# Kernel optimization log

Hardware: AMD Instinct MI355X
Metric: run time of the kernel (lower is better)

The kernel has to match this reference:

```python
import jax, jax.numpy as jnp
import numpy as np

N = 100_000   # nodes
E = 1_600_000 # edges (avg degree 16)
D = 32        # input = hidden = output channels (module defaults)
L = 3         # num_layers


def setup_inputs() -> dict:
    key = jax.random.key(0)
    ks = jax.random.split(key, 6)
    X = jax.random.normal(ks[0], (N, D), jnp.float32)
    edge_index = jax.random.randint(ks[1], (2, E), 0, N)
    edge_weight = jax.random.uniform(ks[2], (E,), jnp.float32)
    # 8 GCNConv layers per GConvLSTM: x_i, h_i, x_f, h_f, x_c, h_c, x_o, h_o
    conv_w = jax.random.normal(ks[3], (L, 8, D, D), jnp.float32) * np.float32(1.0 / np.sqrt(D))
    conv_b = jnp.zeros((L, 8, D), jnp.float32)
    # peephole weights w_c_i, w_c_f, w_c_o (glorot) and biases b_i, b_f, b_c, b_o (zeros)
    wc = jax.random.normal(ks[4], (L, 3, D), jnp.float32) * np.float32(0.1)
    bg = jnp.zeros((L, 4, D), jnp.float32)
    return dict(X=X, edge_index=edge_index, edge_weight=edge_weight,
                conv_w=conv_w, conv_b=conv_b, wc=wc, bg=bg)


def _gcn_norm(edge_index, edge_weight, n):
    # PyG gcn_norm (sym): add self loops with weight 1, then D^-1/2 A D^-1/2
    loop = jnp.arange(n)
    src = jnp.concatenate([edge_index[0], loop])
    dst = jnp.concatenate([edge_index[1], loop])
    w = jnp.concatenate([edge_weight, jnp.ones((n,), edge_weight.dtype)])
    deg = jax.ops.segment_sum(w, dst, num_segments=n)
    dinv = jnp.where(deg > 0, jax.lax.rsqrt(deg), jnp.zeros_like(deg))
    return src, dst, dinv[src] * w * dinv[dst]


def reference(X, edge_index, edge_weight, conv_w, conv_b, wc, bg):
    n = X.shape[0]
    src, dst, nw = _gcn_norm(edge_index, edge_weight, n)

    def gcn(x, W, b):
        xw = x @ W                                   # [N, D] linear transform
        agg = jax.ops.segment_sum(nw[:, None] * xw[src], dst, num_segments=n)
        return agg + b

    out = X
    for l in range(conv_w.shape[0]):
        x = out
        H = jnp.zeros((n, conv_w.shape[-1]), x.dtype)  # hidden state init (None -> zeros)
        C = jnp.zeros_like(H)                          # cell state init
        Wl, bl = conv_w[l], conv_b[l]
        I = jax.nn.sigmoid(gcn(x, Wl[0], bl[0]) + gcn(H, Wl[1], bl[1]) + wc[l, 0] * C + bg[l, 0])
        F = jax.nn.sigmoid(gcn(x, Wl[2], bl[2]) + gcn(H, Wl[3], bl[3]) + wc[l, 1] * C + bg[l, 1])
        T = jnp.tanh(gcn(x, Wl[4], bl[4]) + gcn(H, Wl[5], bl[5]) + bg[l, 2])
        C = F * C + I * T
        O = jax.nn.sigmoid(gcn(x, Wl[6], bl[6]) + gcn(H, Wl[7], bl[7]) + wc[l, 2] * C + bg[l, 3])
        out = O * jnp.tanh(C)
    return out
```

## Files before the change

### kernel.cpp

```cpp
#include <hip/hip_runtime.h>
#include <math.h>

#define TPB 256
#define NBMAX 2048

__device__ __forceinline__ float fsig(float x) {
    return __builtin_amdgcn_rcpf(1.f + __expf(-x));
}
__device__ __forceinline__ float ftanh(float x) {
    float t = __expf(2.f * fabsf(x));
    float r = 1.f - 2.f * __builtin_amdgcn_rcpf(t + 1.f);
    return copysignf(r, x);
}

__global__ __launch_bounds__(256) void k_zero(int* __restrict__ p, int n) {
    int i = blockIdx.x * 256 + threadIdx.x;
    if (i < n) p[i] = 0;
}


__global__ __launch_bounds__(256) void k_bhist(const int* __restrict__ ei,
                                               int* __restrict__ bhist, int E, int NB) {
    __shared__ int h[NBMAX];
    for (int i = threadIdx.x; i < NB; i += 256) h[i] = 0;
    __syncthreads();
    int stride = gridDim.x * 256;
    for (int e = blockIdx.x * 256 + threadIdx.x; e < E; e += stride)
        atomicAdd(&h[ei[E + e] >> 8], 1);
    __syncthreads();
    for (int i = threadIdx.x; i < NB; i += 256) if (h[i]) atomicAdd(&bhist[i], h[i]);
}

__global__ __launch_bounds__(256) void k_bscan(const int* __restrict__ bhist,
                                               int* __restrict__ bbase, int* __restrict__ bfill,
                                               int* __restrict__ row_start,
                                               int NB, int N, int E) {
    __shared__ int tsum[256];
    int tid = threadIdx.x;
    int per = (NB + 255) / 256;
    int loc[8]; int tot = 0;
    int base = tid * per;
#pragma unroll
    for (int j = 0; j < 8; j++) {
        int i = base + j;
        int v = (j < per && i < NB) ? bhist[i] : 0;
        loc[j] = v; tot += v;
    }
    tsum[tid] = tot;
    __syncthreads();
    for (int off = 1; off < 256; off <<= 1) {
        int t = (tid >= off) ? tsum[tid - off] : 0;
        __syncthreads();
        tsum[tid] += t;
        __syncthreads();
    }
    int run = tsum[tid] - tot;
#pragma unroll
    for (int j = 0; j < 8; j++) {
        int i = base + j;
        if (j < per && i < NB) { bbase[i] = run; bfill[i] = run; run += loc[j]; }
    }
    if (tid == 0) { bbase[NB] = E; row_start[N] = E; }
}

__global__ __launch_bounds__(256) void k_bin(const int* __restrict__ ei,
                                             const float* __restrict__ ew,
                                             int* bfill, int2* __restrict__ ebuf,
                                             int E, int NB) {
    __shared__ int h[NBMAX];
    __shared__ int gb[NBMAX];
    const int EPT = 16;
    int tid = threadIdx.x;
    int base = blockIdx.x * 256 * EPT;
    for (int i = tid; i < NB; i += 256) h[i] = 0;
    __syncthreads();
    int src[EPT]; float w[EPT]; int bkt[EPT]; int lrank[EPT];
#pragma unroll
    for (int j = 0; j < EPT; j++) {
        int e = base + j * 256 + tid;
        if (e < E) {
            src[j] = ei[e]; int d = ei[E + e]; w[j] = ew[e];
            int b = d >> 8;
            bkt[j] = b | ((d & 255) << 16);
            lrank[j] = atomicAdd(&h[b], 1);
        } else bkt[j] = -1;
    }
    __syncthreads();
    for (int i = tid; i < NB; i += 256) gb[i] = h[i] ? atomicAdd(&bfill[i], h[i]) : 0;
    __syncthreads();
#pragma unroll
    for (int j = 0; j < EPT; j++) {
        if (bkt[j] >= 0) {
            int b = bkt[j] & 0xFFFF, dlow = (bkt[j] >> 16) & 0xFF;
            int2 v; v.x = src[j] | (dlow << 24); v.y = __float_as_int(w[j]);
            ebuf[gb[b] + lrank[j]] = v;
        }
    }
}

__global__ __launch_bounds__(256) void k_bucket(const int2* __restrict__ ebuf,
                                                const int* __restrict__ bbase,
                                                int2* __restrict__ csr,
                                                int* __restrict__ row_start,
                                                float* __restrict__ dinv,
                                                const float4* __restrict__ X4,
                                                float4* __restrict__ Y4,
                                                int N, int E) {
    __shared__ int lcnt[256];
    __shared__ float wsum[256];
    __shared__ int lstart[256];
    __shared__ int sc[256];
    __shared__ float sdinv[256];
    int b = blockIdx.x, tid = threadIdx.x;
    int beg = bbase[b], end = bbase[b + 1];
    lcnt[tid] = 0; wsum[tid] = 0.f;
    __syncthreads();
    for (int i = beg + tid; i < end; i += 256) {
        int2 v = ebuf[i];
        int dlow = ((unsigned)v.x) >> 24;
        atomicAdd(&lcnt[dlow], 1);
        atomicAdd(&wsum[dlow], __int_as_float(v.y));
    }
    __syncthreads();
    int myc = lcnt[tid];
    sc[tid] = myc;
    __syncthreads();
    for (int off = 1; off < 256; off <<= 1) {
        int t = (tid >= off) ? sc[tid - off] : 0;
        __syncthreads();
        sc[tid] += t;
        __syncthreads();
    }
    lstart[tid] = sc[tid] - myc;
    int node = (b << 8) + tid;
    float dv = rsqrtf(1.0f + wsum[tid]);
    sdinv[tid] = dv;
    if (node < N) {
        row_start[node] = beg + sc[tid] - myc;
        dinv[node] = dv;
    }
    lcnt[tid] = 0;
    __syncthreads();
    for (int i = beg + tid; i < end; i += 256) {
        int2 v = ebuf[i];
        int dlow = ((unsigned)v.x) >> 24;
        int pos = lstart[dlow] + atomicAdd(&lcnt[dlow], 1);
        int2 o; o.x = v.x & 0x00FFFFFF; o.y = v.y;
        csr[beg + pos] = o;
    }
    int nNodes = N - (b << 8); if (nNodes > 256) nNodes = 256;
    int limit = nNodes * 8;
    size_t base4 = ((size_t)b << 8) * 8;
    for (int i = tid; i < limit; i += 256) {
        float4 v = X4[base4 + i];
        float d = sdinv[i >> 3];
        float4 o; o.x = v.x * d; o.y = v.y * d; o.z = v.z * d; o.w = v.w * d;
        Y4[base4 + i] = o;
    }
}


__global__ __launch_bounds__(256) void k_gather(const float4* __restrict__ Y4,
                                                const int* __restrict__ row_start,
                                                const int2* __restrict__ csr,
                                                const float* __restrict__ dinv,
                                                float4* __restrict__ AX4, int N, int E) {
    int wid = (blockIdx.x * blockDim.x + threadIdx.x) >> 6;
    if (wid >= N) return;
    int lane = threadIdx.x & 63;
    int q = lane >> 3, c4 = lane & 7;
    int rs = row_start[wid], re = row_start[wid + 1];
    float di = dinv[wid];
    float4 self = Y4[(size_t)wid * 8 + c4];
    int e0 = rs + q;
    int2 p[4];
#pragma unroll
    for (int j = 0; j < 4; j++) {
        int e = e0 + j * 8;
        p[j] = csr[e < E ? e : 0];
    }
    float4 y[4]; float w[4];
#pragma unroll
    for (int j = 0; j < 4; j++) {
        int e = e0 + j * 8;
        w[j] = (e < re) ? __int_as_float(p[j].y) : 0.f;
        int s = p[j].x;
        y[j] = Y4[(size_t)(e < re ? s : wid) * 8 + c4];
    }
    float4 acc1, acc2;
    if (q == 0) acc1 = self; else { acc1.x = acc1.y = acc1.z = acc1.w = 0.f; }
    acc2.x = acc2.y = acc2.z = acc2.w = 0.f;
    acc1.x += w[0] * y[0].x; acc1.y += w[0] * y[0].y; acc1.z += w[0] * y[0].z; acc1.w += w[0] * y[0].w;
    acc2.x += w[1] * y[1].x; acc2.y += w[1] * y[1].y; acc2.z += w[1] * y[1].z; acc2.w += w[1] * y[1].w;
    acc1.x += w[2] * y[2].x; acc1.y += w[2] * y[2].y; acc1.z += w[2] * y[2].z; acc1.w += w[2] * y[2].w;
    acc2.x += w[3] * y[3].x; acc2.y += w[3] * y[3].y; acc2.z += w[3] * y[3].z; acc2.w += w[3] * y[3].w;
    for (int e = e0 + 32; e < re; e += 8) {
        int2 t = csr[e];
        float4 yt = Y4[(size_t)t.x * 8 + c4];
        float wt = __int_as_float(t.y);
        acc1.x += wt * yt.x; acc1.y += wt * yt.y; acc1.z += wt * yt.z; acc1.w += wt * yt.w;
    }
    acc1.x += acc2.x; acc1.y += acc2.y; acc1.z += acc2.z; acc1.w += acc2.w;
#pragma unroll
    for (int off = 8; off <= 32; off <<= 1) {
        acc1.x += __shfl_xor(acc1.x, off);
        acc1.y += __shfl_xor(acc1.y, off);
        acc1.z += __shfl_xor(acc1.z, off);
        acc1.w += __shfl_xor(acc1.w, off);
    }
    if (lane < 8) {
        float4 o; o.x = acc1.x * di; o.y = acc1.y * di; o.z = acc1.z * di; o.w = acc1.w * di;
        AX4[(size_t)wid * 8 + c4] = o;
    }
}

__global__ __launch_bounds__(256) void k_gates(const float* __restrict__ AX,
                                               const float* __restrict__ cw,
                                               const float* __restrict__ cb,
                                               const float* __restrict__ wc,
                                               const float* __restrict__ bg,
                                               const float* __restrict__ dinv,
                                               float* __restrict__ outRaw,
                                               float* __restrict__ outY,
                                               int N, int l, int isLast) {
    __shared__ float Ws[32][96];
    __shared__ float Xs[32][33];
    __shared__ float Gs[32][96];
    __shared__ float bS[96];
    __shared__ float wcs[32];
    int tid = threadIdx.x;
    for (int i = tid; i < 3072; i += 256) {
        int k = i / 96, ccol = i - k * 96;
        int g = ccol >> 5, o = ccol & 31;
        int j = (g == 0) ? 0 : ((g == 1) ? 4 : 6);
        Ws[k][ccol] = cw[(((l * 8 + j) * 32) + k) * 32 + o];
    }
    if (tid < 32) {
        int c = tid;
        bS[c]      = cb[((l * 8 + 0) * 32) + c] + cb[((l * 8 + 1) * 32) + c] + bg[((l * 4 + 0) * 32) + c];
        bS[32 + c] = cb[((l * 8 + 4) * 32) + c] + cb[((l * 8 + 5) * 32) + c] + bg[((l * 4 + 2) * 32) + c];
        bS[64 + c] = cb[((l * 8 + 6) * 32) + c] + cb[((l * 8 + 7) * 32) + c] + bg[((l * 4 + 3) * 32) + c];
        wcs[c]     = wc[((l * 3 + 2) * 32) + c];
    }
    int row0 = blockIdx.x * 32;
    for (int i = tid; i < 1024; i += 256) {
        int r = i >> 5, k = i & 31; int gr = row0 + r;
        Xs[r][k] = (gr < N) ? AX[(size_t)gr * 32 + k] : 0.f;
    }
    __syncthreads();
    {
        int r = tid >> 3, g8 = tid & 7;
        float acc[12];
#pragma unroll
        for (int j = 0; j < 12; j++) acc[j] = 0.f;
#pragma unroll
        for (int k = 0; k < 32; k++) {
            float xv = Xs[r][k];
#pragma unroll
            for (int j = 0; j < 12; j++) acc[j] += xv * Ws[k][g8 * 12 + j];
        }
#pragma unroll
        for (int j = 0; j < 12; j++) Gs[r][g8 * 12 + j] = acc[j];
    }
    __syncthreads();
    for (int i = tid; i < 1024; i += 256) {
        int r = i >> 5, c = i & 31;
        int gn = row0 + r;
        if (gn >= N) continue;
        float I = fsig(Gs[r][c] + bS[c]);
        float T = ftanh(Gs[r][32 + c] + bS[32 + c]);
        float C = I * T;
        float O = fsig(Gs[r][64 + c] + wcs[c] * C + bS[64 + c]);
        float val = O * ftanh(C);
        if (isLast) outRaw[(size_t)gn * 32 + c] = val;
        else        outY[(size_t)gn * 32 + c] = dinv[gn] * val;
    }
}

extern "C" void kernel_launch(void* const* d_in, const int* in_sizes, int n_in,
                              void* d_out, int out_size, void* d_ws, size_t ws_size,
                              hipStream_t stream) {
    const float* X  = (const float*)d_in[0];
    const int*   ei = (const int*)d_in[1];
    const float* ew = (const float*)d_in[2];
    const float* cw = (const float*)d_in[3];
    const float* cb = (const float*)d_in[4];
    const float* wc = (const float*)d_in[5];
    const float* bg = (const float*)d_in[6];
    int N = in_sizes[0] / 32;
    int E = in_sizes[2];
    int L = in_sizes[3] / (8 * 32 * 32);
    float* out = (float*)d_out;
    int NB = (N + 255) >> 8;

    char* p = (char*)d_ws;
    auto alloc = [&](size_t bytes) -> char* {
        char* r = p; p += (bytes + 255) & ~(size_t)255; return r;
    };
    int*   bhist     = (int*)alloc((size_t)NB * 4);
    int*   bbase     = (int*)alloc((size_t)(NB + 1) * 4);
    int*   bfill     = (int*)alloc((size_t)NB * 4);
    int*   row_start = (int*)alloc((size_t)(N + 1) * 4);
    float* dinv      = (float*)alloc((size_t)N * 4);
    int2*  ebuf      = (int2*)alloc((size_t)E * 8);
    int2*  csr       = (int2*)alloc((size_t)E * 8);
    float* Y         = (float*)alloc((size_t)N * 32 * 4);
    float* AX        = (float*)alloc((size_t)N * 32 * 4);

    k_zero<<<(NB + 255) / 256, 256, 0, stream>>>(bhist, NB);
    k_bhist<<<512, 256, 0, stream>>>(ei, bhist, E, NB);
    k_bscan<<<1, 256, 0, stream>>>(bhist, bbase, bfill, row_start, NB, N, E);
    int nBin = (E + 4095) / 4096;
    k_bin<<<nBin, 256, 0, stream>>>(ei, ew, bfill, ebuf, E, NB);
    k_bucket<<<NB, 256, 0, stream>>>(ebuf, bbase, csr, row_start, dinv,
                                     (const float4*)X, (float4*)Y, N, E);

    for (int l = 0; l < L; l++) {
        k_gather<<<(N + 3) / 4, 256, 0, stream>>>((const float4*)Y, row_start, csr,
                                                  dinv, (float4*)AX, N, E);
        k_gates<<<(N + 31) / 32, 256, 0, stream>>>(AX, cw, cb, wc, bg, dinv,
                                                   out, Y, N, l, l == L - 1);
    }
}
```

Baseline: 262.6 us.

## Rewrite gates kernel as persistent wave-per-node with register-held weights

The gates kernel now launches a fixed grid of 1024 blocks, and each 64-lane wave loops over nodes in a grid-stride pattern. Each lane keeps a weight column for the I/T gate and for the O gate in registers, and broadcasts the node's input features with shuffles instead of staging them through shared memory. The next node's row is prefetched while the current one is computed. This removes the per-block shared-memory tiles and barriers and the repeated weight-tile loads. The cost is 64+ registers per lane for weights and idle O-gate lanes in the upper half of each wave.

```diff
diff --git a/kernel.cpp b/kernel.cpp
--- a/kernel.cpp
+++ b/kernel.cpp
@@ -224,10 +224,6 @@
                                                float* __restrict__ outY,
                                                int N, int l, int isLast) {
     __shared__ float Ws[32][96];
-    __shared__ float Xs[32][33];
-    __shared__ float Gs[32][96];
-    __shared__ float bS[96];
-    __shared__ float wcs[32];
     int tid = threadIdx.x;
     for (int i = tid; i < 3072; i += 256) {
         int k = i / 96, ccol = i - k * 96;
@@ -235,45 +231,47 @@
         int j = (g == 0) ? 0 : ((g == 1) ? 4 : 6);
         Ws[k][ccol] = cw[(((l * 8 + j) * 32) + k) * 32 + o];
     }
-    if (tid < 32) {
-        int c = tid;
-        bS[c]      = cb[((l * 8 + 0) * 32) + c] + cb[((l * 8 + 1) * 32) + c] + bg[((l * 4 + 0) * 32) + c];
-        bS[32 + c] = cb[((l * 8 + 4) * 32) + c] + cb[((l * 8 + 5) * 32) + c] + bg[((l * 4 + 2) * 32) + c];
-        bS[64 + c] = cb[((l * 8 + 6) * 32) + c] + cb[((l * 8 + 7) * 32) + c] + bg[((l * 4 + 3) * 32) + c];
-        wcs[c]     = wc[((l * 3 + 2) * 32) + c];
-    }
-    int row0 = blockIdx.x * 32;
-    for (int i = tid; i < 1024; i += 256) {
-        int r = i >> 5, k = i & 31; int gr = row0 + r;
-        Xs[r][k] = (gr < N) ? AX[(size_t)gr * 32 + k] : 0.f;
-    }
-    __syncthreads();
-    {
-        int r = tid >> 3, g8 = tid & 7;
-        float acc[12];
-#pragma unroll
-        for (int j = 0; j < 12; j++) acc[j] = 0.f;
+    __syncthreads();
+    int lane = tid & 63;
+    int c = lane & 31, g = lane >> 5;
+    float wg[32], wo[32];
+#pragma unroll
+    for (int k = 0; k < 32; k++) wg[k] = Ws[k][g * 32 + c];
+#pragma unroll
+    for (int k = 0; k < 32; k++) wo[k] = Ws[k][64 + c];
+    float bGc = (g == 0)
+        ? cb[((l * 8 + 0) * 32) + c] + cb[((l * 8 + 1) * 32) + c] + bg[((l * 4 + 0) * 32) + c]
+        : cb[((l * 8 + 4) * 32) + c] + cb[((l * 8 + 5) * 32) + c] + bg[((l * 4 + 2) * 32) + c];
+    float bOc = cb[((l * 8 + 6) * 32) + c] + cb[((l * 8 + 7) * 32) + c] + bg[((l * 4 + 3) * 32) + c];
+    float wcc = wc[((l * 3 + 2) * 32) + c];
+
+    int wgid = (blockIdx.x * blockDim.x + tid) >> 6;
+    int nwaves = (gridDim.x * blockDim.x) >> 6;
+    int n = wgid;
+    float rv = 0.f, dv = 0.f;
+    if (n < N) { rv = AX[(size_t)n * 32 + c]; dv = dinv[n]; }
+    for (; n < N; ) {
+        int n2 = n + nwaves;
+        float rv2 = 0.f, dv2 = 0.f;
+        if (n2 < N) { rv2 = AX[(size_t)n2 * 32 + c]; dv2 = dinv[n2]; }
+        float ag = 0.f, ao = 0.f;
 #pragma unroll
         for (int k = 0; k < 32; k++) {
-            float xv = Xs[r][k];
-#pragma unroll
-            for (int j = 0; j < 12; j++) acc[j] += xv * Ws[k][g8 * 12 + j];
+            float rk = __shfl(rv, k);
+            ag += rk * wg[k];
+            ao += rk * wo[k];
         }
-#pragma unroll
-        for (int j = 0; j < 12; j++) Gs[r][g8 * 12 + j] = acc[j];
-    }
-    __syncthreads();
-    for (int i = tid; i < 1024; i += 256) {
-        int r = i >> 5, c = i & 31;
-        int gn = row0 + r;
-        if (gn >= N) continue;
-        float I = fsig(Gs[r][c] + bS[c]);
-        float T = ftanh(Gs[r][32 + c] + bS[32 + c]);
-        float C = I * T;
-        float O = fsig(Gs[r][64 + c] + wcs[c] * C + bS[64 + c]);
-        float val = O * ftanh(C);
-        if (isLast) outRaw[(size_t)gn * 32 + c] = val;
-        else        outY[(size_t)gn * 32 + c] = dinv[gn] * val;
+        float tpre = __shfl(ag, lane | 32);
+        if (lane < 32) {
+            float I = fsig(ag + bGc);
+            float T = ftanh(tpre + __shfl(bGc, lane | 32));
+            float C = I * T;
+            float O = fsig(ao + wcc * C + bOc);
+            float val = O * ftanh(C);
+            if (isLast) outRaw[(size_t)n * 32 + c] = val;
+            else        outY[(size_t)n * 32 + c] = dv * val;
+        }
+        n = n2; rv = rv2; dv = dv2;
     }
 }
 
@@ -318,7 +316,7 @@
     for (int l = 0; l < L; l++) {
         k_gather<<<(N + 3) / 4, 256, 0, stream>>>((const float4*)Y, row_start, csr,
                                                   dinv, (float4*)AX, N, E);
-        k_gates<<<(N + 31) / 32, 256, 0, stream>>>(AX, cw, cb, wc, bg, dinv,
-                                                   out, Y, N, l, l == L - 1);
-    }
-}
+        k_gates<<<1024, 256, 0, stream>>>(AX, cw, cb, wc, bg, dinv,
+                                          out, Y, N, l, l == L - 1);
+    }
+}
```

Result: slower. 316.3 us (+20.5%).

## Register-tile gate GEMM over 128 rows and fuse activation without shared staging

Applied to the files above, without the earlier changes.

The gate kernel now handles 128 rows per block instead of 32. Each thread keeps a 4-row by 4-column tile for all three gates in registers and reads weights as float4, so the gate activations run straight from registers. This removes the Gs shared-memory round trip and a barrier, amortises the per-block weight load over more rows, and writes the outputs as float4. In exchange each thread holds more registers and the grid has fewer blocks.

```diff
diff --git a/kernel.cpp b/kernel.cpp
--- a/kernel.cpp
+++ b/kernel.cpp
@@ -224,10 +224,10 @@
                                                float* __restrict__ outY,
                                                int N, int l, int isLast) {
     __shared__ float Ws[32][96];
-    __shared__ float Xs[32][33];
-    __shared__ float Gs[32][96];
+    __shared__ float Xs[128][33];
     __shared__ float bS[96];
     __shared__ float wcs[32];
+    __shared__ float sdv[128];
     int tid = threadIdx.x;
     for (int i = tid; i < 3072; i += 256) {
         int k = i / 96, ccol = i - k * 96;
@@ -242,38 +242,56 @@
         bS[64 + c] = cb[((l * 8 + 6) * 32) + c] + cb[((l * 8 + 7) * 32) + c] + bg[((l * 4 + 3) * 32) + c];
         wcs[c]     = wc[((l * 3 + 2) * 32) + c];
     }
-    int row0 = blockIdx.x * 32;
-    for (int i = tid; i < 1024; i += 256) {
+    int row0 = blockIdx.x * 128;
+    for (int i = tid; i < 4096; i += 256) {
         int r = i >> 5, k = i & 31; int gr = row0 + r;
         Xs[r][k] = (gr < N) ? AX[(size_t)gr * 32 + k] : 0.f;
     }
-    __syncthreads();
-    {
-        int r = tid >> 3, g8 = tid & 7;
-        float acc[12];
-#pragma unroll
-        for (int j = 0; j < 12; j++) acc[j] = 0.f;
-#pragma unroll
-        for (int k = 0; k < 32; k++) {
-            float xv = Xs[r][k];
-#pragma unroll
-            for (int j = 0; j < 12; j++) acc[j] += xv * Ws[k][g8 * 12 + j];
+    if (tid < 128) {
+        int gr = row0 + tid;
+        sdv[tid] = (gr < N) ? dinv[gr] : 0.f;
+    }
+    __syncthreads();
+    int r0 = tid >> 3, g8 = tid & 7, cbase = g8 * 4;
+    float aI[4][4], aT[4][4], aO[4][4];
+#pragma unroll
+    for (int j = 0; j < 4; j++)
+#pragma unroll
+        for (int cc = 0; cc < 4; cc++) { aI[j][cc] = 0.f; aT[j][cc] = 0.f; aO[j][cc] = 0.f; }
+#pragma unroll 4
+    for (int k = 0; k < 32; k++) {
+        float4 wI = *(const float4*)&Ws[k][cbase];
+        float4 wT = *(const float4*)&Ws[k][32 + cbase];
+        float4 wO = *(const float4*)&Ws[k][64 + cbase];
+#pragma unroll
+        for (int j = 0; j < 4; j++) {
+            float xv = Xs[r0 + 32 * j][k];
+            aI[j][0] += xv * wI.x; aI[j][1] += xv * wI.y; aI[j][2] += xv * wI.z; aI[j][3] += xv * wI.w;
+            aT[j][0] += xv * wT.x; aT[j][1] += xv * wT.y; aT[j][2] += xv * wT.z; aT[j][3] += xv * wT.w;
+            aO[j][0] += xv * wO.x; aO[j][1] += xv * wO.y; aO[j][2] += xv * wO.z; aO[j][3] += xv * wO.w;
         }
-#pragma unroll
-        for (int j = 0; j < 12; j++) Gs[r][g8 * 12 + j] = acc[j];
-    }
-    __syncthreads();
-    for (int i = tid; i < 1024; i += 256) {
-        int r = i >> 5, c = i & 31;
+    }
+#pragma unroll
+    for (int j = 0; j < 4; j++) {
+        int r = r0 + 32 * j;
         int gn = row0 + r;
         if (gn >= N) continue;
-        float I = fsig(Gs[r][c] + bS[c]);
-        float T = ftanh(Gs[r][32 + c] + bS[32 + c]);
-        float C = I * T;
-        float O = fsig(Gs[r][64 + c] + wcs[c] * C + bS[64 + c]);
-        float val = O * ftanh(C);
-        if (isLast) outRaw[(size_t)gn * 32 + c] = val;
-        else        outY[(size_t)gn * 32 + c] = dinv[gn] * val;
+        float di = sdv[r];
+        float4 v;
+        float res[4];
+#pragma unroll
+        for (int cc = 0; cc < 4; cc++) {
+            int c = cbase + cc;
+            float I = fsig(aI[j][cc] + bS[c]);
+            float T = ftanh(aT[j][cc] + bS[32 + c]);
+            float C = I * T;
+            float O = fsig(aO[j][cc] + wcs[c] * C + bS[64 + c]);
+            float val = O * ftanh(C);
+            res[cc] = isLast ? val : di * val;
+        }
+        v.x = res[0]; v.y = res[1]; v.z = res[2]; v.w = res[3];
+        float* dst = isLast ? outRaw : outY;
+        *(float4*)&dst[(size_t)gn * 32 + cbase] = v;
     }
 }
 
@@ -318,7 +336,7 @@
     for (int l = 0; l < L; l++) {
         k_gather<<<(N + 3) / 4, 256, 0, stream>>>((const float4*)Y, row_start, csr,
                                                   dinv, (float4*)AX, N, E);
-        k_gates<<<(N + 31) / 32, 256, 0, stream>>>(AX, cw, cb, wc, bg, dinv,
-                                                   out, Y, N, l, l == L - 1);
-    }
-}
+        k_gates<<<(N + 127) / 128, 256, 0, stream>>>(AX, cw, cb, wc, bg, dinv,
+                                                     out, Y, N, l, l == L - 1);
+    }
+}
```

After: 250.2 us. -4.7%, faster.
